# Kernel tuning notes

Hardware: AMD Instinct MI355X
Metric: run time of the kernel (lower is better)

The kernel has to match this reference:

```python
import jax, jax.numpy as jnp
import numpy as np

DIM = 768
NH = 12
HD = DIM // NH  # 64, also the depthwise-pool channel count
SR = 2
EPS_SRN = 1e-6   # sr_norm / up_norm eps
EPS_LN = 1e-5    # default nn.LayerNorm eps for norm_q/k/v


def ln(x, g, b, eps):
    m = x.mean(-1, keepdims=True)
    v = x.var(-1, keepdims=True)
    return (x - m) / jnp.sqrt(v + eps) * g + b


def dwconv(x, w, stride, pad, bias=None):
    # x [N,C,H,W], w [C*m,1,kh,kw] (torch depthwise layout), groups = C
    y = jax.lax.conv_general_dilated(
        x, w, (stride, stride), [(pad, pad), (pad, pad)],
        feature_group_count=x.shape[1],
        dimension_numbers=('NCHW', 'OIHW', 'NCHW'))
    return y if bias is None else y + bias[None, :, None, None]


def setup_inputs() -> dict:
    key = jax.random.key(0)
    ks = jax.random.split(key, 8)
    B, H, W = 8, 56, 56
    N = H * W
    s = 0.02
    f32 = jnp.float32
    d = {
        'x': jax.random.normal(ks[0], (B, N, DIM), f32),
        'q_w': jax.random.normal(ks[1], (DIM, DIM), f32) * s,
        'q_b': jnp.zeros((DIM,), f32),
        'kv_w': jax.random.normal(ks[2], (DIM, 2 * DIM), f32) * s,
        'kv_b': jnp.zeros((2 * DIM,), f32),
        'sr_w': jax.random.normal(ks[3], (DIM, 1, 3, 3), f32) * s,
        'sr_b': jnp.zeros((DIM,), f32),
        'srn_g': jnp.ones((DIM,), f32), 'srn_b': jnp.zeros((DIM,), f32),
        'up_w': jax.random.normal(ks[4], (SR * SR * DIM, 1, 3, 3), f32) * s,
        'up_b': jnp.zeros((SR * SR * DIM,), f32),
        'upn_g': jnp.ones((DIM,), f32), 'upn_b': jnp.zeros((DIM,), f32),
        'proj_w': jax.random.normal(ks[5], (DIM, DIM), f32) * s,
        'proj_b': jnp.zeros((DIM,), f32),
        'pq_w': jax.random.normal(ks[6], (HD, 1, 3, 3), f32) * s,
        'pk_w': jax.random.normal(ks[7], (HD, 1, 3, 3), f32) * s,
        'pv_w': jax.random.normal(jax.random.fold_in(key, 7), (HD, 1, 3, 3), f32) * s,
        'nq_g': jnp.ones((HD,), f32), 'nq_b': jnp.zeros((HD,), f32),
        'nk_g': jnp.ones((HD,), f32), 'nk_b': jnp.zeros((HD,), f32),
        'nv_g': jnp.ones((HD,), f32), 'nv_b': jnp.zeros((HD,), f32),
        'H': H, 'W': W,
    }
    return d


def _forward(x, q_w, q_b, kv_w, kv_b, sr_w, sr_b, srn_g, srn_b,
             up_w, up_b, upn_g, upn_b, proj_w, proj_b,
             pq_w, pk_w, pv_w, nq_g, nq_b, nk_g, nk_b, nv_g, nv_b, H, W):
    B, N, C = x.shape
    scale = HD ** -0.5
    # q projection -> [B, NH, N, HD]
    q = (x @ q_w + q_b).reshape(B, N, NH, HD).transpose(0, 2, 1, 3)
    # pool_q: per-head depthwise 3x3 stride-1 conv + LayerNorm(HD)
    qi = q.reshape(B * NH, H, W, HD).transpose(0, 3, 1, 2)
    qi = dwconv(qi, pq_w, 1, 1)
    q = qi.reshape(B, NH, HD, H * W).transpose(0, 1, 3, 2)
    q = ln(q, nq_g, nq_b, EPS_LN)
    # spatial reduction of x (depthwise k=3, s=2, p=1) + LayerNorm
    xs = x.transpose(0, 2, 1).reshape(B, C, H, W)
    xs = dwconv(xs, sr_w, SR, SR // 2, sr_b)
    Hs, Ws = xs.shape[2], xs.shape[3]  # H//SR, W//SR
    xs = xs.reshape(B, C, Hs * Ws).transpose(0, 2, 1)
    xs = ln(xs, srn_g, srn_b, EPS_SRN)
    # kv projection -> k, v [B, NH, Hs*Ws, HD]
    kv = (xs @ kv_w + kv_b).reshape(B, Hs * Ws, 2, NH, HD).transpose(2, 0, 3, 1, 4)
    k, v = kv[0], kv[1]

    def pool_kv(t, w, g, b):
        ti = t.reshape(B * NH, Hs, Ws, HD).transpose(0, 3, 1, 2)
        ti = dwconv(ti, w, 2, 1)  # stride_kv=(2,2), pad 1
        hk, wk = ti.shape[2], ti.shape[3]
        t2 = ti.reshape(B, NH, HD, hk * wk).transpose(0, 1, 3, 2)
        return ln(t2, g, b, EPS_LN)

    kp = pool_kv(k, pk_w, nk_g, nk_b)
    vp = pool_kv(v, pv_w, nv_g, nv_b)
    # attention core
    attn = jax.nn.softmax(jnp.einsum('bhnd,bhmd->bhnm', q, kp) * scale, axis=-1)
    out = jnp.einsum('bhnm,bhmd->bhnd', attn, vp).transpose(0, 2, 1, 3).reshape(B, N, C)
    # identity path: unpooled v -> depthwise conv -> PixelShuffle(SR) upsample
    idn = v.transpose(0, 1, 3, 2).reshape(B, C, Hs, Ws)
    idn = dwconv(idn, up_w, 1, 1, up_b)  # [B, SR*SR*C, Hs, Ws], groups=C
    idn = idn.reshape(B, C, SR, SR, Hs, Ws).transpose(0, 1, 4, 2, 5, 3).reshape(B, C, Hs * SR, Ws * SR)
    idn = idn.reshape(B, C, N).transpose(0, 2, 1)
    idn = ln(idn, upn_g, upn_b, EPS_SRN)
    return (out + idn) @ proj_w + proj_b


def reference(x, q_w, q_b, kv_w, kv_b, sr_w, sr_b, srn_g, srn_b,
              up_w, up_b, upn_g, upn_b, proj_w, proj_b,
              pq_w, pk_w, pv_w, nq_g, nq_b, nk_g, nk_b, nv_g, nv_b, H, W):
    return _forward(x, q_w, q_b, kv_w, kv_b, sr_w, sr_b, srn_g, srn_b,
                    up_w, up_b, upn_g, upn_b, proj_w, proj_b,
                    pq_w, pk_w, pv_w, nq_g, nq_b, nk_g, nk_b, nv_g, nv_b, H, W)
```

## Files before the change

kernel.cpp:

```cpp
#include <hip/hip_runtime.h>
#include <cstdint>
#include <cstddef>

#define DIM 768
#define NHD 12
#define HD  64
#define HH  56
#define WW  56
#define NQ  3136
#define HS  28
#define WSS 28
#define NS  784
#define HK  14
#define WK  14
#define NKK 196
#define NKP 224
#define VSTR 256

typedef __bf16 bf16x8 __attribute__((ext_vector_type(8)));
typedef __bf16 bf16x4 __attribute__((ext_vector_type(4)));
typedef float  f32x4  __attribute__((ext_vector_type(4)));

__device__ __forceinline__ int xcd_swizzle(int bid, int nwg) {
  const int q = nwg >> 3, r = nwg & 7;
  const int xcd = bid & 7, off = bid >> 3;
  return (xcd < r ? xcd * (q + 1) : r * (q + 1) + (xcd - r) * q) + off;
}

__device__ __forceinline__ void gload_lds16(const void* g, void* l) {
  __builtin_amdgcn_global_load_lds(
      (const __attribute__((address_space(1))) void*)g,
      (__attribute__((address_space(3))) void*)l, 16, 0, 0);
}

__device__ __forceinline__ unsigned pack_bf2(float a, float b) {
  union { __bf16 h; unsigned short u; } lo, hi;
  lo.h = (__bf16)a; hi.h = (__bf16)b;
  return (unsigned)lo.u | ((unsigned)hi.u << 16);
}

#define LDP 40

template<int MODE>
__global__ __launch_bounds__(256) void gemm_mfma_kernel(
    const __bf16* __restrict__ A, const __bf16* __restrict__ Bt,
    const float* __restrict__ bias, float* __restrict__ C,
    __bf16* __restrict__ Cq, int M, int N, int K)
{
  __shared__ __bf16 As[128 * LDP];
  __shared__ __bf16 Bs[128 * LDP];

  const int nX = N >> 7;
  const int bid = xcd_swizzle(blockIdx.x, (M >> 7) * nX);
  const int row0 = (bid / nX) << 7;
  const int col0 = (bid % nX) << 7;

  const int t = threadIdx.x;
  const int lane = t & 63;
  const int w = t >> 6;
  const int wr = w >> 1, wc = w & 1;

  const int rs = t >> 1;
  const int kh = (t & 1) << 4;
  const __bf16* Aptr = A + (size_t)(row0 + rs) * K + kh;
  const __bf16* Bptr = Bt + (size_t)(col0 + rs) * K + kh;

  f32x4 acc[4][4];
#pragma unroll
  for (int i = 0; i < 4; ++i)
#pragma unroll
    for (int j = 0; j < 4; ++j) acc[i][j] = (f32x4){0.f, 0.f, 0.f, 0.f};

  const int fr = lane & 15;
  const int fc = lane >> 4;

  int4 a0 = *(const int4*)(Aptr);
  int4 a1 = *(const int4*)(Aptr + 8);
  int4 b0 = *(const int4*)(Bptr);
  int4 b1 = *(const int4*)(Bptr + 8);

  const int NT = K >> 5;
  for (int kt = 0; kt < NT; ++kt) {
    __syncthreads();
    *(int4*)(&As[rs * LDP + kh]) = a0;
    *(int4*)(&As[rs * LDP + kh + 8]) = a1;
    *(int4*)(&Bs[rs * LDP + kh]) = b0;
    *(int4*)(&Bs[rs * LDP + kh + 8]) = b1;
    __syncthreads();
    if (kt + 1 < NT) {
      const __bf16* ap = Aptr + ((kt + 1) << 5);
      const __bf16* bp = Bptr + ((kt + 1) << 5);
      a0 = *(const int4*)(ap);
      a1 = *(const int4*)(ap + 8);
      b0 = *(const int4*)(bp);
      b1 = *(const int4*)(bp + 8);
    }
    bf16x8 af[4], bfr[4];
#pragma unroll
    for (int i = 0; i < 4; ++i)
      af[i] = *(const bf16x8*)(&As[(wr * 64 + i * 16 + fr) * LDP + fc * 8]);
#pragma unroll
    for (int j = 0; j < 4; ++j)
      bfr[j] = *(const bf16x8*)(&Bs[(wc * 64 + j * 16 + fr) * LDP + fc * 8]);
#pragma unroll
    for (int i = 0; i < 4; ++i)
#pragma unroll
      for (int j = 0; j < 4; ++j)
        acc[i][j] = __builtin_amdgcn_mfma_f32_16x16x32_bf16(af[i], bfr[j], acc[i][j], 0, 0, 0);
  }

  const int orow = row0 + wr * 64 + ((lane >> 4) << 2);
  const int ocol = col0 + wc * 64 + (lane & 15);
#pragma unroll
  for (int j = 0; j < 4; ++j) {
    const int col = ocol + j * 16;
    const float bv = bias[col];
#pragma unroll
    for (int i = 0; i < 4; ++i)
#pragma unroll
      for (int r = 0; r < 4; ++r) {
        const int rrow = orow + i * 16 + r;
        if (MODE == 0) {
          C[(size_t)rrow * N + col] = acc[i][j][r] + bv;
        } else if (MODE == 1) {
          const int b = rrow / NQ, n = rrow - b * NQ;
          const int h = col >> 6, hd = col & 63;
          Cq[(((size_t)b * NHD + h) * NQ + n) * HD + hd] = (__bf16)(acc[i][j][r] + bv);
        } else {
          Cq[(size_t)rrow * N + col] = (__bf16)(acc[i][j][r] + bv);
        }
      }
  }
}

__global__ __launch_bounds__(256) void cast_bf16_kernel(
    const float* __restrict__ in, __bf16* __restrict__ out, long n4)
{
  long i = (long)blockIdx.x * 256 + threadIdx.x;
  const long stride = (long)gridDim.x * 256;
  for (; i < n4; i += stride) {
    float4 v = *(const float4*)(in + i * 4);
    bf16x4 o;
    o.x = (__bf16)v.x; o.y = (__bf16)v.y; o.z = (__bf16)v.z; o.w = (__bf16)v.w;
    *(bf16x4*)(out + i * 4) = o;
  }
}

__global__ __launch_bounds__(256) void wt_cast_kernel(
    const float* __restrict__ W, __bf16* __restrict__ Wt, int K, int N)
{
  __shared__ float tile[32][33];
  const int k0 = blockIdx.y << 5;
  const int n0 = blockIdx.x << 5;
  const int tc = threadIdx.x & 31;
  const int tr = threadIdx.x >> 5;
#pragma unroll
  for (int i = 0; i < 4; ++i)
    tile[tr + i * 8][tc] = W[(size_t)(k0 + tr + i * 8) * N + n0 + tc];
  __syncthreads();
#pragma unroll
  for (int i = 0; i < 4; ++i)
    Wt[(size_t)(n0 + tr + i * 8) * K + k0 + tc] = (__bf16)tile[tc][tr + i * 8];
}

__global__ __launch_bounds__(256) void up_tr_kernel(
    const float* __restrict__ upw, float* __restrict__ upt)
{
  const int i = blockIdx.x * 256 + threadIdx.x;
  if (i < 4 * 9 * DIM) {
    const int c = i % DIM;
    const int rest = i / DIM;
    const int tap = rest % 9, sidx = rest / 9;
    upt[i] = upw[(c * 4 + sidx) * 9 + tap];
  }
}

__global__ __launch_bounds__(256) void sr_tr_kernel(
    const float* __restrict__ srw, float* __restrict__ srt)
{
  const int i = blockIdx.x * 256 + threadIdx.x;
  if (i < 9 * DIM) {
    const int c = i % DIM;
    const int tap = i / DIM;
    srt[i] = srw[c * 9 + tap];
  }
}

__global__ __launch_bounds__(256) void pool_q_ln_kernel(
    const __bf16* __restrict__ qp, const float* __restrict__ pqw,
    const float* __restrict__ g, const float* __restrict__ bb,
    __bf16* __restrict__ qf)
{
  const int blk = xcd_swizzle(blockIdx.x, gridDim.x);
  const int bh = blk / HH, y = blk - bh * HH;
  const int lane = threadIdx.x & 63;
  const int w = threadIdx.x >> 6;
  const int x0 = w * (WW / 4);

  float wt[9];
#pragma unroll
  for (int tap = 0; tap < 9; ++tap) {
    const int yy = y - 1 + tap / 3;
    wt[tap] = (yy >= 0 && yy < HH) ? pqw[lane * 9 + tap] : 0.f;
  }
  const float gl = g[lane], bl = bb[lane];

  const __bf16* rp0;
  const __bf16* rp1;
  const __bf16* rp2;
  {
    const __bf16* base = qp + (size_t)bh * NQ * HD + lane;
    rp0 = base + (size_t)min(max(y - 1, 0), HH - 1) * WW * HD;
    rp1 = base + (size_t)y * WW * HD;
    rp2 = base + (size_t)min(max(y + 1, 0), HH - 1) * WW * HD;
  }
  auto ldc = [&](int xx, float* d) {
    const float m = (xx >= 0 && xx < WW) ? 1.f : 0.f;
    const int xc = min(max(xx, 0), WW - 1);
    d[0] = m * (float)rp0[(size_t)xc * HD];
    d[1] = m * (float)rp1[(size_t)xc * HD];
    d[2] = m * (float)rp2[(size_t)xc * HD];
  };

  float c0[3], c1[3], c2[3], cn[3];
  ldc(x0 - 1, c0);
  ldc(x0,     c1);
  ldc(x0 + 1, c2);

#pragma unroll
  for (int xi = 0; xi < WW / 4; ++xi) {
    const int x = x0 + xi;
    ldc(x + 2, cn);
    float acc = 0.f;
#pragma unroll
    for (int dy = 0; dy < 3; ++dy) {
      acc = fmaf(wt[dy * 3 + 0], c0[dy], acc);
      acc = fmaf(wt[dy * 3 + 1], c1[dy], acc);
      acc = fmaf(wt[dy * 3 + 2], c2[dy], acc);
    }
    float s = acc, sq = acc * acc;
#pragma unroll
    for (int off = 32; off > 0; off >>= 1) {
      s  += __shfl_xor(s, off);
      sq += __shfl_xor(sq, off);
    }
    const float mean = s * (1.f / 64.f);
    const float var  = sq * (1.f / 64.f) - mean * mean;
    const float rstd = rsqrtf(var + 1e-5f);
    qf[((size_t)bh * NQ + y * WW + x) * HD + lane] =
        (__bf16)((acc - mean) * rstd * gl + bl);
#pragma unroll
    for (int dy = 0; dy < 3; ++dy) {
      c0[dy] = c1[dy]; c1[dy] = c2[dy]; c2[dy] = cn[dy];
    }
  }
}

__global__ __launch_bounds__(256) void sr_ln_kernel(
    const __bf16* __restrict__ x, const float* __restrict__ srt,
    const float* __restrict__ srb, const float* __restrict__ g,
    const float* __restrict__ bb, __bf16* __restrict__ out)
{
  const int row = xcd_swizzle(blockIdx.x, gridDim.x);
  const int b = row / NS, ns = row - b * NS;
  const int ys = ns / WSS, xs = ns - ys * WSS;
  const int t = threadIdx.x;

  float fm[9];
  size_t off9[9];
#pragma unroll
  for (int tap = 0; tap < 9; ++tap) {
    const int yy = 2 * ys - 1 + tap / 3;
    const int xx = 2 * xs - 1 + tap % 3;
    fm[tap] = (yy >= 0 && yy < HH && xx >= 0 && xx < WW) ? 1.f : 0.f;
    const int yyc = min(max(yy, 0), HH - 1);
    const int xxc = min(max(xx, 0), WW - 1);
    off9[tap] = ((size_t)b * NQ + yyc * WW + xxc) * DIM;
  }

  float vals[3];
  float lsum = 0.f, lsq = 0.f;
#pragma unroll
  for (int i = 0; i < 3; ++i) {
    const int c = t + i * 256;
    float v9[9];
#pragma unroll
    for (int tap = 0; tap < 9; ++tap) v9[tap] = (float)x[off9[tap] + c];
    float acc = srb[c];
#pragma unroll
    for (int tap = 0; tap < 9; ++tap)
      acc = fmaf(srt[tap * DIM + c] * fm[tap], v9[tap], acc);
    vals[i] = acc;
    lsum += acc;
    lsq = fmaf(acc, acc, lsq);
  }
#pragma unroll
  for (int off = 32; off > 0; off >>= 1) {
    lsum += __shfl_xor(lsum, off);
    lsq  += __shfl_xor(lsq, off);
  }
  __shared__ float s1[4], s2[4];
  if ((t & 63) == 0) { s1[t >> 6] = lsum; s2[t >> 6] = lsq; }
  __syncthreads();
  const float S  = s1[0] + s1[1] + s1[2] + s1[3];
  const float SQ = s2[0] + s2[1] + s2[2] + s2[3];
  const float mean = S * (1.f / 768.f);
  const float var  = SQ * (1.f / 768.f) - mean * mean;
  const float rstd = rsqrtf(var + 1e-6f);
#pragma unroll
  for (int i = 0; i < 3; ++i) {
    const int c = t + i * 256;
    out[(size_t)row * DIM + c] = (__bf16)((vals[i] - mean) * rstd * g[c] + bb[c]);
  }
}

__global__ __launch_bounds__(256) void pool_kv_ln_kernel(
    const __bf16* __restrict__ kv, const float* __restrict__ pkw,
    const float* __restrict__ pvw, const float* __restrict__ kg,
    const float* __restrict__ kbb, const float* __restrict__ vg,
    const float* __restrict__ vbb, __bf16* __restrict__ kpb,
    __bf16* __restrict__ vtb)
{
  const int isv = blockIdx.y;
  const float* pw = isv ? pvw : pkw;
  const float* g  = isv ? vg  : kg;
  const float* bb = isv ? vbb : kbb;
  const int coloff = isv ? DIM : 0;

  const int lane = threadIdx.x & 63;
  const int r = blockIdx.x * 4 + (threadIdx.x >> 6);
  const int bh = r / NKP;
  const int nk = r - bh * NKP;

  float val = 0.f;
  if (nk < NKK) {
    const int b = bh / NHD, h = bh - b * NHD;
    const int yk = nk / WK, xk = nk - yk * WK;
    float acc = 0.f;
#pragma unroll
    for (int dy = 0; dy < 3; ++dy) {
      const int yy = 2 * yk - 1 + dy;
      if (yy < 0 || yy >= HS) continue;
#pragma unroll
      for (int dx = 0; dx < 3; ++dx) {
        const int xx = 2 * xk - 1 + dx;
        if (xx < 0 || xx >= WSS) continue;
        acc = fmaf(pw[lane * 9 + dy * 3 + dx],
                   (float)kv[((size_t)b * NS + yy * WSS + xx) * (2 * DIM) + coloff + h * HD + lane], acc);
      }
    }
    float s = acc, sq = acc * acc;
#pragma unroll
    for (int off = 32; off > 0; off >>= 1) {
      s  += __shfl_xor(s, off);
      sq += __shfl_xor(sq, off);
    }
    const float mean = s * (1.f / 64.f);
    const float var  = sq * (1.f / 64.f) - mean * mean;
    const float rstd = rsqrtf(var + 1e-5f);
    val = (acc - mean) * rstd * g[lane] + bb[lane];
  }
  if (!isv) {
    kpb[(size_t)bh * NKP * HD + nk * HD + (lane ^ ((nk & 7) << 3))] = (__bf16)val;
  } else {
    vtb[(size_t)bh * HD * VSTR + lane * VSTR + (nk ^ ((lane & 7) << 3))] = (__bf16)val;
  }
}

__global__ __launch_bounds__(256) void attn_mfma_kernel(
    const __bf16* __restrict__ qf, const __bf16* __restrict__ kpb,
    const __bf16* __restrict__ vtb, __bf16* __restrict__ out)
{
  __shared__ __bf16 kv_lds[16384];
  const int bh = blockIdx.y;
  const int qt = blockIdx.x;
  const int t = threadIdx.x;
  const int lane = t & 63, w = t >> 6;
  const int fr = lane & 15;
  const int fg = lane >> 4;
  const int q0 = qt * 64 + w * 16;
  const int sw = (fr & 7) << 4;

  const __bf16* qbase = qf + ((size_t)bh * NQ + q0) * HD;
  const bf16x8 aq0 = *(const bf16x8*)(qbase + fr * HD + fg * 8);
  const bf16x8 aq1 = *(const bf16x8*)(qbase + fr * HD + 32 + fg * 8);

  char* kl = (char*)kv_lds;
  {
    const __bf16* kgp = kpb + (size_t)bh * (NKP * HD);
#pragma unroll
    for (int i = 0; i < 7; ++i)
      gload_lds16(kgp + (i * 256 + w * 64 + lane) * 8, kl + i * 4096 + w * 1024);
  }
  __syncthreads();

  f32x4 s[13];
#pragma unroll
  for (int n = 0; n < 13; ++n) {
    const int rowb = (n * 16 + fr) << 7;
    const bf16x8 b0 = *(const bf16x8*)(kl + rowb + ((fg << 4) ^ sw));
    const bf16x8 b1 = *(const bf16x8*)(kl + rowb + (((fg << 4) + 64) ^ sw));
    f32x4 c = (f32x4){0.f, 0.f, 0.f, 0.f};
    c = __builtin_amdgcn_mfma_f32_16x16x32_bf16(b0, aq0, c, 0, 0, 0);
    c = __builtin_amdgcn_mfma_f32_16x16x32_bf16(b1, aq1, c, 0, 0, 0);
    s[n] = c;
  }
  __syncthreads();

  {
    const __bf16* vgp = vtb + (size_t)bh * (HD * VSTR);
#pragma unroll
    for (int i = 0; i < 8; ++i)
      gload_lds16(vgp + (i * 256 + w * 64 + lane) * 8, kl + i * 4096 + w * 1024);
  }

  const float scale = 0.125f;
  unsigned pk[28];
  float sum = 0.f;
#pragma unroll
  for (int n = 0; n < 13; ++n) {
    float e0 = __expf(s[n][0] * scale);
    float e1 = __expf(s[n][1] * scale);
    float e2 = __expf(s[n][2] * scale);
    float e3 = __expf(s[n][3] * scale);
    if (n == 12 && fg >= 1) { e0 = e1 = e2 = e3 = 0.f; }
    sum += (e0 + e1) + (e2 + e3);
    pk[2 * n]     = pack_bf2(e0, e1);
    pk[2 * n + 1] = pack_bf2(e2, e3);
  }
  pk[26] = 0u; pk[27] = 0u;
  sum += __shfl_xor(sum, 16);
  sum += __shfl_xor(sum, 32);
  const float pinvL = 1.f / sum;

  __syncthreads();

  const int L1 = ((fg & 1) << 5) | fr;
  const int L2 = L1 + 16;
  const bool hi = (fg >= 2);
  f32x4 acc2[4];
#pragma unroll
  for (int dt = 0; dt < 4; ++dt) acc2[dt] = (f32x4){0.f, 0.f, 0.f, 0.f};
  const char* vl = (const char*)kv_lds;
#pragma unroll
  for (int ks = 0; ks < 7; ++ks) {
    const unsigned d0a = __shfl(pk[4 * ks + 0], L1), d0b = __shfl(pk[4 * ks + 2], L1);
    const unsigned d1a = __shfl(pk[4 * ks + 1], L1), d1b = __shfl(pk[4 * ks + 3], L1);
    const unsigned d2a = __shfl(pk[4 * ks + 0], L2), d2b = __shfl(pk[4 * ks + 2], L2);
    const unsigned d3a = __shfl(pk[4 * ks + 1], L2), d3b = __shfl(pk[4 * ks + 3], L2);
    uint4 pu;
    pu.x = hi ? d0b : d0a;
    pu.y = hi ? d1b : d1a;
    pu.z = hi ? d2b : d2a;
    pu.w = hi ? d3b : d3a;
    const bf16x8 pabf = __builtin_bit_cast(bf16x8, pu);
#pragma unroll
    for (int dt = 0; dt < 4; ++dt) {
      const bf16x8 bv = *(const bf16x8*)(vl + (dt * 16 + fr) * (VSTR * 2) + ((ks * 64 + (fg << 4)) ^ sw));
      acc2[dt] = __builtin_amdgcn_mfma_f32_16x16x32_bf16(pabf, bv, acc2[dt], 0, 0, 0);
    }
  }

  float pr[4];
#pragma unroll
  for (int r = 0; r < 4; ++r)
    pr[r] = __shfl(pinvL, (fg << 4) | (fg * 4 + r));
  const int b = bh / NHD, h = bh - b * NHD;
#pragma unroll
  for (int dt = 0; dt < 4; ++dt)
#pragma unroll
    for (int r = 0; r < 4; ++r)
      out[((size_t)b * NQ + q0 + 4 * fg + r) * DIM + h * HD + dt * 16 + fr] =
          (__bf16)(acc2[dt][r] * pr[r]);
}

#define XCH 2

__global__ __launch_bounds__(256) void idn_add_ln_kernel(
    const __bf16* __restrict__ kv, const float* __restrict__ upt,
    const float* __restrict__ upb, const float* __restrict__ g,
    const float* __restrict__ bb, const __bf16* __restrict__ io,
    __bf16* __restrict__ pj)
{
  int idx = xcd_swizzle(blockIdx.x, gridDim.x);
  const int chunk = idx & (XCH - 1); idx >>= 1;
  const int ys = idx % HS; idx /= HS;
  const int sidx = idx & 3;
  const int b = idx >> 2;
  const int sy = sidx >> 1, sx = sidx & 1;
  const int y = 2 * ys + sy;
  const int t = threadIdx.x;
  const int w = t >> 6;

  float wreg[3][9], ubias[3], gg[3], gb[3];
#pragma unroll
  for (int i = 0; i < 3; ++i) {
    const int c = t + i * 256;
    ubias[i] = upb[c * 4 + sidx];
    gg[i] = g[c];
    gb[i] = bb[c];
#pragma unroll
    for (int tap = 0; tap < 9; ++tap) {
      const int yy = ys - 1 + tap / 3;
      const float f = (yy >= 0 && yy < HS) ? 1.f : 0.f;
      wreg[i][tap] = upt[(sidx * 9 + tap) * DIM + c] * f;
    }
  }

  __shared__ __bf16 vals_lds[14][DIM];
  __shared__ float s1[14][4], s2[14][4];
  const int xs0 = chunk * 14;

  const int y0 = max(ys - 1, 0), y1 = ys, y2 = min(ys + 1, HS - 1);
  const __bf16* vb0 = kv + ((size_t)(b * NS + y0 * WSS)) * (2 * DIM) + DIM + t;
  const __bf16* vb1 = kv + ((size_t)(b * NS + y1 * WSS)) * (2 * DIM) + DIM + t;
  const __bf16* vb2 = kv + ((size_t)(b * NS + y2 * WSS)) * (2 * DIM) + DIM + t;

  auto ldcol = [&](int ch, int p, float* dst) {
    const float m = (p >= 0 && p < WSS) ? 1.f : 0.f;
    const int xx = min(max(p, 0), WSS - 1);
    const size_t off = (size_t)xx * (2 * DIM) + ch * 256;
    dst[0] = m * (float)vb0[off];
    dst[1] = m * (float)vb1[off];
    dst[2] = m * (float)vb2[off];
  };

  float c0[3][3], c1[3][3], c2[3][3], cn[3][3];
#pragma unroll
  for (int ch = 0; ch < 3; ++ch) {
    ldcol(ch, xs0 - 1, c0[ch]);
    ldcol(ch, xs0,     c1[ch]);
    ldcol(ch, xs0 + 1, c2[ch]);
  }

#pragma unroll
  for (int xi = 0; xi < 14; ++xi) {
    const int xs = xs0 + xi;
#pragma unroll
    for (int ch = 0; ch < 3; ++ch) ldcol(ch, xs + 2, cn[ch]);
    float lsum = 0.f, lsq = 0.f;
#pragma unroll
    for (int ch = 0; ch < 3; ++ch) {
      float acc = ubias[ch];
#pragma unroll
      for (int dy = 0; dy < 3; ++dy) {
        acc = fmaf(wreg[ch][dy * 3 + 0], c0[ch][dy], acc);
        acc = fmaf(wreg[ch][dy * 3 + 1], c1[ch][dy], acc);
        acc = fmaf(wreg[ch][dy * 3 + 2], c2[ch][dy], acc);
      }
      vals_lds[xi][t + ch * 256] = (__bf16)acc;
      lsum += acc;
      lsq = fmaf(acc, acc, lsq);
    }
#pragma unroll
    for (int off = 32; off > 0; off >>= 1) {
      lsum += __shfl_xor(lsum, off);
      lsq  += __shfl_xor(lsq, off);
    }
    if ((t & 63) == 0) { s1[xi][w] = lsum; s2[xi][w] = lsq; }
#pragma unroll
    for (int ch = 0; ch < 3; ++ch)
#pragma unroll
      for (int dy = 0; dy < 3; ++dy) {
        c0[ch][dy] = c1[ch][dy];
        c1[ch][dy] = c2[ch][dy];
        c2[ch][dy] = cn[ch][dy];
      }
  }
  __syncthreads();

#pragma unroll
  for (int xi = 0; xi < 14; ++xi) {
    const float S  = s1[xi][0] + s1[xi][1] + s1[xi][2] + s1[xi][3];
    const float SQ = s2[xi][0] + s2[xi][1] + s2[xi][2] + s2[xi][3];
    const float mean = S * (1.f / 768.f);
    const float var  = SQ * (1.f / 768.f) - mean * mean;
    const float rstd = rsqrtf(var + 1e-6f);
    const int x = 2 * (xs0 + xi) + sx;
    const size_t row = (size_t)b * NQ + y * WW + x;
#pragma unroll
    for (int ch = 0; ch < 3; ++ch) {
      const int c = t + ch * 256;
      pj[row * DIM + c] =
          (__bf16)((float)io[row * DIM + c] +
                   ((float)vals_lds[xi][c] - mean) * rstd * gg[ch] + gb[ch]);
    }
  }
}

extern "C" void kernel_launch(void* const* d_in, const int* in_sizes, int n_in,
                              void* d_out, int out_size, void* d_ws, size_t ws_size,
                              hipStream_t stream)
{
  const float* x      = (const float*)d_in[0];
  const float* q_w    = (const float*)d_in[1];
  const float* q_b    = (const float*)d_in[2];
  const float* kv_w   = (const float*)d_in[3];
  const float* kv_b   = (const float*)d_in[4];
  const float* sr_w   = (const float*)d_in[5];
  const float* sr_b   = (const float*)d_in[6];
  const float* srn_g  = (const float*)d_in[7];
  const float* srn_b  = (const float*)d_in[8];
  const float* up_w   = (const float*)d_in[9];
  const float* up_b   = (const float*)d_in[10];
  const float* upn_g  = (const float*)d_in[11];
  const float* upn_b  = (const float*)d_in[12];
  const float* proj_w = (const float*)d_in[13];
  const float* proj_b = (const float*)d_in[14];
  const float* pq_w   = (const float*)d_in[15];
  const float* pk_w   = (const float*)d_in[16];
  const float* pv_w   = (const float*)d_in[17];
  const float* nq_g   = (const float*)d_in[18];
  const float* nq_b   = (const float*)d_in[19];
  const float* nk_g   = (const float*)d_in[20];
  const float* nk_b   = (const float*)d_in[21];
  const float* nv_g   = (const float*)d_in[22];
  const float* nv_b   = (const float*)d_in[23];

  const int B = in_sizes[0] / (NQ * DIM);
  const int M1 = B * NQ;
  const int M2 = B * NS;

  char* p = (char*)d_ws;
  __bf16* xb    = (__bf16*)p;  p += (size_t)M1 * DIM * 2;
  float*  qproj = (float*)p;   p += (size_t)M1 * DIM * 4;
  __bf16* qf    = (__bf16*)p;  p += (size_t)M1 * DIM * 2;
  __bf16* xsln  = (__bf16*)p;  p += (size_t)M2 * DIM * 2;
  __bf16* kvb   = (__bf16*)p;  p += (size_t)M2 * 2 * DIM * 2;
  __bf16* kpb   = (__bf16*)p;  p += (size_t)B * NHD * NKP * HD * 2;
  __bf16* vtb   = (__bf16*)p;  p += (size_t)B * NHD * HD * VSTR * 2;
  __bf16* wqt   = (__bf16*)p;  p += (size_t)DIM * DIM * 2;
  __bf16* wkvt  = (__bf16*)p;  p += (size_t)DIM * 2 * DIM * 2;
  __bf16* wpjt  = (__bf16*)p;  p += (size_t)DIM * DIM * 2;
  float*  upt   = (float*)p;   p += (size_t)4 * 9 * DIM * 4;
  float*  srt   = (float*)p;   p += (size_t)9 * DIM * 4;
  __bf16* qp      = (__bf16*)qproj;
  __bf16* attnout = (__bf16*)qproj;
  __bf16* pjin    = xb;

  dim3 blk(256);

  cast_bf16_kernel<<<2048, blk, 0, stream>>>(x, xb, (long)M1 * DIM / 4);
  wt_cast_kernel<<<dim3(DIM / 32, DIM / 32), blk, 0, stream>>>(q_w, wqt, DIM, DIM);
  wt_cast_kernel<<<dim3(2 * DIM / 32, DIM / 32), blk, 0, stream>>>(kv_w, wkvt, DIM, 2 * DIM);
  wt_cast_kernel<<<dim3(DIM / 32, DIM / 32), blk, 0, stream>>>(proj_w, wpjt, DIM, DIM);
  up_tr_kernel<<<(4 * 9 * DIM + 255) / 256, blk, 0, stream>>>(up_w, upt);
  sr_tr_kernel<<<(9 * DIM + 255) / 256, blk, 0, stream>>>(sr_w, srt);

  gemm_mfma_kernel<1><<<(M1 / 128) * (DIM / 128), blk, 0, stream>>>(
      xb, wqt, q_b, nullptr, qp, M1, DIM, DIM);

  pool_q_ln_kernel<<<B * NHD * HH, blk, 0, stream>>>(
      qp, pq_w, nq_g, nq_b, qf);

  sr_ln_kernel<<<B * NS, blk, 0, stream>>>(
      xb, srt, sr_b, srn_g, srn_b, xsln);

  gemm_mfma_kernel<2><<<(M2 / 128) * (2 * DIM / 128), blk, 0, stream>>>(
      xsln, wkvt, kv_b, nullptr, kvb, M2, 2 * DIM, DIM);

  pool_kv_ln_kernel<<<dim3((B * NHD * NKP) / 4, 2), blk, 0, stream>>>(
      kvb, pk_w, pv_w, nk_g, nk_b, nv_g, nv_b, kpb, vtb);

  attn_mfma_kernel<<<dim3(NQ / 64, B * NHD), blk, 0, stream>>>(
      qf, kpb, vtb, attnout);

  idn_add_ln_kernel<<<B * 4 * HS * XCH, blk, 0, stream>>>(
      kvb, upt, up_b, upn_g, upn_b, attnout, pjin);

  gemm_mfma_kernel<0><<<(M1 / 128) * (DIM / 128), blk, 0, stream>>>(
      pjin, wpjt, proj_b, (float*)d_out, nullptr, M1, DIM, DIM);
}
```

Before: 329.3 us.

## Double-buffer GEMM tiles via direct global-to-LDS loads and merge weight-prep launches

The GEMM kernel now stages A/B tiles with global_load_lds directly into double-buffered, XOR-swizzled LDS instead of going through registers into padded LDS. This removes one of the two barriers per k-step and overlaps the next tile's load with the current MFMA work. Separately, the three weight transpose-casts are merged into one launch and the two conv-weight transposes into another, which cuts launch overhead. The risk is that the swizzle must match the read pattern exactly, and the tighter pipeline depends on the async LDS loads finishing before the single barrier.

```diff
diff --git a/kernel.cpp b/kernel.cpp
--- a/kernel.cpp
+++ b/kernel.cpp
@@ -39,16 +39,14 @@
   return (unsigned)lo.u | ((unsigned)hi.u << 16);
 }
 
-#define LDP 40
-
 template<int MODE>
 __global__ __launch_bounds__(256) void gemm_mfma_kernel(
     const __bf16* __restrict__ A, const __bf16* __restrict__ Bt,
     const float* __restrict__ bias, float* __restrict__ C,
     __bf16* __restrict__ Cq, int M, int N, int K)
 {
-  __shared__ __bf16 As[128 * LDP];
-  __shared__ __bf16 Bs[128 * LDP];
+  __shared__ __bf16 As[2][128 * 32];
+  __shared__ __bf16 Bs[2][128 * 32];
 
   const int nX = N >> 7;
   const int bid = xcd_swizzle(blockIdx.x, (M >> 7) * nX);
@@ -59,54 +57,68 @@
   const int lane = t & 63;
   const int w = t >> 6;
   const int wr = w >> 1, wc = w & 1;
-
-  const int rs = t >> 1;
-  const int kh = (t & 1) << 4;
-  const __bf16* Aptr = A + (size_t)(row0 + rs) * K + kh;
-  const __bf16* Bptr = Bt + (size_t)(col0 + rs) * K + kh;
-
-  f32x4 acc[4][4];
-#pragma unroll
-  for (int i = 0; i < 4; ++i)
-#pragma unroll
-    for (int j = 0; j < 4; ++j) acc[i][j] = (f32x4){0.f, 0.f, 0.f, 0.f};
-
   const int fr = lane & 15;
   const int fc = lane >> 4;
 
-  int4 a0 = *(const int4*)(Aptr);
-  int4 a1 = *(const int4*)(Aptr + 8);
-  int4 b0 = *(const int4*)(Bptr);
-  int4 b1 = *(const int4*)(Bptr + 8);
+  const int r0 = t >> 2;
+  const int ch = t & 3;
+  const int sc = ch ^ ((r0 >> 1) & 3);
+  const __bf16* Ap0 = A + (size_t)(row0 + r0) * K + sc * 8;
+  const __bf16* Ap1 = A + (size_t)(row0 + r0 + 64) * K + sc * 8;
+  const __bf16* Bp0 = Bt + (size_t)(col0 + r0) * K + sc * 8;
+  const __bf16* Bp1 = Bt + (size_t)(col0 + r0 + 64) * K + sc * 8;
+  char* Asb = (char*)As;
+  char* Bsb = (char*)Bs;
+  const int db = w * 1024;
+
+  f32x4 acc[4][4];
+#pragma unroll
+  for (int i = 0; i < 4; ++i)
+#pragma unroll
+    for (int j = 0; j < 4; ++j) acc[i][j] = (f32x4){0.f, 0.f, 0.f, 0.f};
+
+  const int keyA = (fr >> 1) & 3;
 
   const int NT = K >> 5;
+
+  {
+    gload_lds16(Ap0, Asb + db);
+    gload_lds16(Ap1, Asb + 4096 + db);
+    gload_lds16(Bp0, Bsb + db);
+    gload_lds16(Bp1, Bsb + 4096 + db);
+  }
+  __syncthreads();
+
+  int cur = 0;
   for (int kt = 0; kt < NT; ++kt) {
-    __syncthreads();
-    *(int4*)(&As[rs * LDP + kh]) = a0;
-    *(int4*)(&As[rs * LDP + kh + 8]) = a1;
-    *(int4*)(&Bs[rs * LDP + kh]) = b0;
-    *(int4*)(&Bs[rs * LDP + kh + 8]) = b1;
-    __syncthreads();
     if (kt + 1 < NT) {
-      const __bf16* ap = Aptr + ((kt + 1) << 5);
-      const __bf16* bp = Bptr + ((kt + 1) << 5);
-      a0 = *(const int4*)(ap);
-      a1 = *(const int4*)(ap + 8);
-      b0 = *(const int4*)(bp);
-      b1 = *(const int4*)(bp + 8);
-    }
+      const int ko = (kt + 1) << 5;
+      const int ob = (cur ^ 1) * 8192;
+      gload_lds16(Ap0 + ko, Asb + ob + db);
+      gload_lds16(Ap1 + ko, Asb + ob + 4096 + db);
+      gload_lds16(Bp0 + ko, Bsb + ob + db);
+      gload_lds16(Bp1 + ko, Bsb + ob + 4096 + db);
+    }
+    const char* Ab = Asb + cur * 8192;
+    const char* Bb = Bsb + cur * 8192;
     bf16x8 af[4], bfr[4];
 #pragma unroll
-    for (int i = 0; i < 4; ++i)
-      af[i] = *(const bf16x8*)(&As[(wr * 64 + i * 16 + fr) * LDP + fc * 8]);
-#pragma unroll
-    for (int j = 0; j < 4; ++j)
-      bfr[j] = *(const bf16x8*)(&Bs[(wc * 64 + j * 16 + fr) * LDP + fc * 8]);
+    for (int i = 0; i < 4; ++i) {
+      const int r = wr * 64 + i * 16 + fr;
+      af[i] = *(const bf16x8*)(Ab + r * 64 + ((fc ^ keyA) << 4));
+    }
+#pragma unroll
+    for (int j = 0; j < 4; ++j) {
+      const int r = wc * 64 + j * 16 + fr;
+      bfr[j] = *(const bf16x8*)(Bb + r * 64 + ((fc ^ keyA) << 4));
+    }
 #pragma unroll
     for (int i = 0; i < 4; ++i)
 #pragma unroll
       for (int j = 0; j < 4; ++j)
         acc[i][j] = __builtin_amdgcn_mfma_f32_16x16x32_bf16(af[i], bfr[j], acc[i][j], 0, 0, 0);
+    __syncthreads();
+    cur ^= 1;
   }
 
   const int orow = row0 + wr * 64 + ((lane >> 4) << 2);
@@ -146,12 +158,19 @@
   }
 }
 
-__global__ __launch_bounds__(256) void wt_cast_kernel(
-    const float* __restrict__ W, __bf16* __restrict__ Wt, int K, int N)
-{
+__global__ __launch_bounds__(256) void wt3_cast_kernel(
+    const float* __restrict__ q_w, const float* __restrict__ kv_w,
+    const float* __restrict__ proj_w, __bf16* __restrict__ wqt,
+    __bf16* __restrict__ wkvt, __bf16* __restrict__ wpjt)
+{
+  const int which = blockIdx.z;
+  const float* W = (which == 0) ? q_w : (which == 1) ? kv_w : proj_w;
+  __bf16* Wt = (which == 0) ? wqt : (which == 1) ? wkvt : wpjt;
+  const int N = (which == 1) ? 2 * DIM : DIM;
+  const int n0 = blockIdx.x << 5;
+  if (n0 >= N) return;
+  const int k0 = blockIdx.y << 5;
   __shared__ float tile[32][33];
-  const int k0 = blockIdx.y << 5;
-  const int n0 = blockIdx.x << 5;
   const int tc = threadIdx.x & 31;
   const int tr = threadIdx.x >> 5;
 #pragma unroll
@@ -160,11 +179,12 @@
   __syncthreads();
 #pragma unroll
   for (int i = 0; i < 4; ++i)
-    Wt[(size_t)(n0 + tr + i * 8) * K + k0 + tc] = (__bf16)tile[tc][tr + i * 8];
-}
-
-__global__ __launch_bounds__(256) void up_tr_kernel(
-    const float* __restrict__ upw, float* __restrict__ upt)
+    Wt[(size_t)(n0 + tr + i * 8) * DIM + k0 + tc] = (__bf16)tile[tc][tr + i * 8];
+}
+
+__global__ __launch_bounds__(256) void misc_tr_kernel(
+    const float* __restrict__ upw, float* __restrict__ upt,
+    const float* __restrict__ srw, float* __restrict__ srt)
 {
   const int i = blockIdx.x * 256 + threadIdx.x;
   if (i < 4 * 9 * DIM) {
@@ -172,17 +192,13 @@
     const int rest = i / DIM;
     const int tap = rest % 9, sidx = rest / 9;
     upt[i] = upw[(c * 4 + sidx) * 9 + tap];
-  }
-}
-
-__global__ __launch_bounds__(256) void sr_tr_kernel(
-    const float* __restrict__ srw, float* __restrict__ srt)
-{
-  const int i = blockIdx.x * 256 + threadIdx.x;
-  if (i < 9 * DIM) {
-    const int c = i % DIM;
-    const int tap = i / DIM;
-    srt[i] = srw[c * 9 + tap];
+  } else {
+    const int j = i - 4 * 9 * DIM;
+    if (j < 9 * DIM) {
+      const int c = j % DIM;
+      const int tap = j / DIM;
+      srt[j] = srw[c * 9 + tap];
+    }
   }
 }
 
@@ -641,11 +657,10 @@
   dim3 blk(256);
 
   cast_bf16_kernel<<<2048, blk, 0, stream>>>(x, xb, (long)M1 * DIM / 4);
-  wt_cast_kernel<<<dim3(DIM / 32, DIM / 32), blk, 0, stream>>>(q_w, wqt, DIM, DIM);
-  wt_cast_kernel<<<dim3(2 * DIM / 32, DIM / 32), blk, 0, stream>>>(kv_w, wkvt, DIM, 2 * DIM);
-  wt_cast_kernel<<<dim3(DIM / 32, DIM / 32), blk, 0, stream>>>(proj_w, wpjt, DIM, DIM);
-  up_tr_kernel<<<(4 * 9 * DIM + 255) / 256, blk, 0, stream>>>(up_w, upt);
-  sr_tr_kernel<<<(9 * DIM + 255) / 256, blk, 0, stream>>>(sr_w, srt);
+  wt3_cast_kernel<<<dim3(48, 24, 3), blk, 0, stream>>>(
+      q_w, kv_w, proj_w, wqt, wkvt, wpjt);
+  misc_tr_kernel<<<(5 * 9 * DIM + 255) / 256, blk, 0, stream>>>(
+      up_w, upt, sr_w, srt);
 
   gemm_mfma_kernel<1><<<(M1 / 128) * (DIM / 128), blk, 0, stream>>>(
       xb, wqt, q_b, nullptr, qp, M1, DIM, DIM);
```

Measured after the change: 320.0 us. 1.03x faster.
